# Performance work log

Measured on AMD Instinct MI355X. Metric: run time of the kernel, lower is better.

The kernel has to match this reference:

```python
import jax, jax.numpy as jnp
import numpy as np

TAU = 0.05
SIGMA = 0.05
THETA = 1.0
MAX_ITER = 30
B, N, M1, M2 = 8192, 256, 128, 64


def setup_inputs() -> dict:
    key = jax.random.key(0)
    k = jax.random.split(key, 5)
    x0 = jax.random.normal(k[0], (B, N), dtype=jnp.float32)
    y1_0 = jnp.zeros((B, M1), dtype=jnp.float32)
    y2_0 = jnp.zeros((B, M2), dtype=jnp.float32)
    z = jax.random.normal(k[1], (B, M1 + M2), dtype=jnp.float32)
    c = jax.random.normal(k[2], (N,), dtype=jnp.float32)
    # scale constraint matrices so tau*sigma*||A||^2 < 1 (PDHG stability)
    A1 = jax.random.normal(k[3], (M1, N), dtype=jnp.float32) * 0.1
    A2 = jax.random.normal(k[4], (M2, N), dtype=jnp.float32) * 0.1
    return {"x0": x0, "y1_0": y1_0, "y2_0": y2_0, "z": z, "c": c, "A1": A1, "A2": A2}


def reference(x0, y1_0, y2_0, z, c, A1, A2):
    # affine constraint maps: ineq_map(x, z) = x @ A1^T - z1 ; eq_map(x, z) = x @ A2^T - z2
    # adjoints: A1^T y1 = y1 @ A1 ; A2^T y2 = y2 @ A2
    # prox: projection onto nonnegative orthant
    z1, z2 = z[:, :M1], z[:, M1:]

    def step(carry, _):
        x, x_bar, y1, y2 = carry
        y1 = jnp.maximum(y1 + SIGMA * (x_bar @ A1.T - z1), 0.0)   # dual ineq ascent + clamp
        y2 = y2 + SIGMA * (x_bar @ A2.T - z2)                     # dual eq ascent
        grad = c + y1 @ A1 + y2 @ A2                              # [B, N] via broadcast of c
        x_next = jnp.maximum(x - TAU * grad, 0.0)                 # prox (nonneg projection)
        x_bar = x_next + THETA * (x_next - x)                     # extrapolation
        return (x_next, x_bar, y1, y2), None

    (x, _, y1, y2), _ = jax.lax.scan(step, (x0, x0, y1_0, y2_0), None, length=MAX_ITER)
    return (x, y1, y2)
```

## Files before the change

### kernel.cpp

```cpp
#include <hip/hip_runtime.h>

typedef __attribute__((ext_vector_type(8))) __bf16 bf16x8;
typedef __attribute__((ext_vector_type(4))) float f32x4;

constexpr int Bn = 8192, Nn = 256, M1n = 128, M2n = 64, Mn = 192, ITERS = 30;
constexpr float TAUc = 0.05f, SIGc = 0.05f;

__device__ __forceinline__ ushort f2bf(float f) {
  unsigned u = __builtin_bit_cast(unsigned, f);
  u = (u + 0x7FFFu + ((u >> 16) & 1u)) >> 16;
  return (ushort)u;
}

__device__ __forceinline__ unsigned cvtpk(float lo, float hi) {
  unsigned r;
  asm("v_cvt_pk_bf16_f32 %0, %1, %2" : "=v"(r) : "v"(lo), "v"(hi));
  return r;
}

__global__ void prep_kernel(const float* __restrict__ A1, const float* __restrict__ A2,
                            ushort* __restrict__ Arm, ushort* __restrict__ AT) {
  int i = blockIdx.x * 256 + threadIdx.x;
  if (i >= Mn * Nn) return;
  int m = i / Nn, n = i % Nn;
  float v = (m < M1n) ? A1[m * Nn + n] : A2[(m - M1n) * Nn + n];
  ushort b = f2bf(v);
  Arm[m * Nn + n] = b;
  AT[n * Mn + m] = b;
}

__global__ __launch_bounds__(256, 2) void pdhg_kernel(
    const float* __restrict__ x0, const float* __restrict__ y10,
    const float* __restrict__ y20, const float* __restrict__ z,
    const float* __restrict__ c, const ushort* __restrict__ Arm,
    const ushort* __restrict__ AT, float* __restrict__ out) {
  __shared__ __align__(16) ushort xb_lds[16][264];
  __shared__ __align__(16) ushort y_lds[16][200];
  __shared__ __align__(16) float z_lds[16][200];

  const int lane = threadIdx.x & 63;
  const int w = threadIdx.x >> 6;
  const int fr = lane & 15;
  const int kg = lane >> 4;
  const int row0 = blockIdx.x * 16;

  for (int idx = threadIdx.x; idx < 16 * Mn; idx += 256) {
    int r = idx / Mn, m = idx - r * Mn;
    z_lds[r][m] = SIGc * z[(row0 + r) * Mn + m];
  }

  float x[4][4], cv[4], ys[3][4];

#pragma unroll
  for (int t = 0; t < 4; ++t) {
    int n = (4 * w + t) * 16 + fr;
    cv[t] = c[n];
#pragma unroll
    for (int g = 0; g < 4; ++g) {
      float v = x0[(row0 + kg * 4 + g) * Nn + n];
      x[t][g] = v;
      xb_lds[kg * 4 + g][n] = f2bf(v);
    }
  }
#pragma unroll
  for (int i = 0; i < 3; ++i) {
    int mt = 3 * w + i;
    int m = mt * 16 + fr;
#pragma unroll
    for (int g = 0; g < 4; ++g) {
      int r = row0 + kg * 4 + g;
      ys[i][g] = (m < M1n) ? y10[r * M1n + m] : y20[r * M2n + (m - M1n)];
    }
  }

  bf16x8 armF[3][8], atF[4][6];
#pragma unroll
  for (int i = 0; i < 3; ++i) {
    int m = (3 * w + i) * 16 + fr;
#pragma unroll
    for (int kf = 0; kf < 8; ++kf)
      armF[i][kf] = *reinterpret_cast<const bf16x8*>(&Arm[m * Nn + kf * 32 + kg * 8]);
  }
#pragma unroll
  for (int t = 0; t < 4; ++t) {
    int n = (4 * w + t) * 16 + fr;
#pragma unroll
    for (int kf = 0; kf < 6; ++kf)
      atF[t][kf] = *reinterpret_cast<const bf16x8*>(&AT[n * Mn + kf * 32 + kg * 8]);
  }

  __syncthreads();

  for (int it = 0; it < ITERS; ++it) {
    f32x4 a0 = {0.f, 0.f, 0.f, 0.f}, a1 = a0, a2 = a0;
#pragma unroll
    for (int kf = 0; kf < 8; ++kf) {
      bf16x8 fx = *reinterpret_cast<const bf16x8*>(&xb_lds[fr][kf * 32 + kg * 8]);
      a0 = __builtin_amdgcn_mfma_f32_16x16x32_bf16(fx, armF[0][kf], a0, 0, 0, 0);
      a1 = __builtin_amdgcn_mfma_f32_16x16x32_bf16(fx, armF[1][kf], a1, 0, 0, 0);
      a2 = __builtin_amdgcn_mfma_f32_16x16x32_bf16(fx, armF[2][kf], a2, 0, 0, 0);
    }

#pragma unroll
    for (int i = 0; i < 3; ++i) {
      int mt = 3 * w + i;
      int m = mt * 16 + fr;
      const f32x4 ai = (i == 0) ? a0 : (i == 1) ? a1 : a2;
#pragma unroll
      for (int g = 0; g < 4; ++g) {
        float s = __builtin_fmaf(SIGc, ai[g], ys[i][g]) - z_lds[kg * 4 + g][m];
        if (mt < 8) s = fmaxf(s, 0.f);
        ys[i][g] = s;
      }
      unsigned p01 = cvtpk(ys[i][0], ys[i][1]);
      unsigned p23 = cvtpk(ys[i][2], ys[i][3]);
      y_lds[kg * 4 + 0][m] = (ushort)p01;
      y_lds[kg * 4 + 1][m] = (ushort)(p01 >> 16);
      y_lds[kg * 4 + 2][m] = (ushort)p23;
      y_lds[kg * 4 + 3][m] = (ushort)(p23 >> 16);
    }
    __syncthreads();

    f32x4 b0 = {0.f, 0.f, 0.f, 0.f}, b1 = b0, b2 = b0, b3 = b0;
#pragma unroll
    for (int kf = 0; kf < 6; ++kf) {
      bf16x8 fy = *reinterpret_cast<const bf16x8*>(&y_lds[fr][kf * 32 + kg * 8]);
      b0 = __builtin_amdgcn_mfma_f32_16x16x32_bf16(fy, atF[0][kf], b0, 0, 0, 0);
      b1 = __builtin_amdgcn_mfma_f32_16x16x32_bf16(fy, atF[1][kf], b1, 0, 0, 0);
      b2 = __builtin_amdgcn_mfma_f32_16x16x32_bf16(fy, atF[2][kf], b2, 0, 0, 0);
      b3 = __builtin_amdgcn_mfma_f32_16x16x32_bf16(fy, atF[3][kf], b3, 0, 0, 0);
    }

    const bool notlast = (it != ITERS - 1);
#pragma unroll
    for (int t = 0; t < 4; ++t) {
      int n = (4 * w + t) * 16 + fr;
      const f32x4 bt = (t == 0) ? b0 : (t == 1) ? b1 : (t == 2) ? b2 : b3;
      float xb[4];
#pragma unroll
      for (int g = 0; g < 4; ++g) {
        float grad = cv[t] + bt[g];
        float xn = fmaxf(__builtin_fmaf(-TAUc, grad, x[t][g]), 0.f);
        xb[g] = 2.f * xn - x[t][g];
        x[t][g] = xn;
      }
      if (notlast) {
        unsigned p01 = cvtpk(xb[0], xb[1]);
        unsigned p23 = cvtpk(xb[2], xb[3]);
        xb_lds[kg * 4 + 0][n] = (ushort)p01;
        xb_lds[kg * 4 + 1][n] = (ushort)(p01 >> 16);
        xb_lds[kg * 4 + 2][n] = (ushort)p23;
        xb_lds[kg * 4 + 3][n] = (ushort)(p23 >> 16);
      }
    }
    if (notlast) __syncthreads();
  }

  float* ox = out;
  float* oy1 = out + Bn * Nn;
  float* oy2 = oy1 + Bn * M1n;
#pragma unroll
  for (int t = 0; t < 4; ++t) {
    int n = (4 * w + t) * 16 + fr;
#pragma unroll
    for (int g = 0; g < 4; ++g)
      ox[(row0 + kg * 4 + g) * Nn + n] = x[t][g];
  }
#pragma unroll
  for (int i = 0; i < 3; ++i) {
    int m = (3 * w + i) * 16 + fr;
#pragma unroll
    for (int g = 0; g < 4; ++g) {
      int r = row0 + kg * 4 + g;
      if (m < M1n) oy1[r * M1n + m] = ys[i][g];
      else         oy2[r * M2n + (m - M1n)] = ys[i][g];
    }
  }
}

extern "C" void kernel_launch(void* const* d_in, const int* in_sizes, int n_in,
                              void* d_out, int out_size, void* d_ws, size_t ws_size,
                              hipStream_t stream) {
  const float* x0  = (const float*)d_in[0];
  const float* y10 = (const float*)d_in[1];
  const float* y20 = (const float*)d_in[2];
  const float* z   = (const float*)d_in[3];
  const float* c   = (const float*)d_in[4];
  const float* A1  = (const float*)d_in[5];
  const float* A2  = (const float*)d_in[6];

  ushort* Arm = (ushort*)d_ws;
  ushort* AT  = Arm + Mn * Nn;

  prep_kernel<<<(Mn * Nn + 255) / 256, 256, 0, stream>>>(A1, A2, Arm, AT);
  pdhg_kernel<<<Bn / 16, 256, 0, stream>>>(x0, y10, y20, z, c, Arm, AT, (float*)d_out);
}
```

Measured before the change: 81.81 us.

## Process two 16-row batches per block with matrix fragments pinned in AGPRs

Each block now handles 32 batch rows as two 16-row sub-tiles that share the register-resident A and A^T fragments, halving the number of blocks and the per-block fragment loads. The fragments are forced into accumulation registers through inline asm, and MFMAs take their B operand from AGPRs, freeing VGPRs for the doubled x/y state. Issuing two independent MFMA streams per barrier phase gives more instruction-level parallelism, but occupancy drops to one block per CU and only 256 blocks remain, which may underfill the GPU.

```diff
diff --git a/kernel.cpp b/kernel.cpp
--- a/kernel.cpp
+++ b/kernel.cpp
@@ -2,6 +2,7 @@
 
 typedef __attribute__((ext_vector_type(8))) __bf16 bf16x8;
 typedef __attribute__((ext_vector_type(4))) float f32x4;
+typedef __attribute__((ext_vector_type(4))) int i32x4;
 
 constexpr int Bn = 8192, Nn = 256, M1n = 128, M2n = 64, Mn = 192, ITERS = 30;
 constexpr float TAUc = 0.05f, SIGc = 0.05f;
@@ -16,6 +17,12 @@
   unsigned r;
   asm("v_cvt_pk_bf16_f32 %0, %1, %2" : "=v"(r) : "v"(lo), "v"(hi));
   return r;
+}
+
+__device__ __forceinline__ void pina(i32x4& v) { asm volatile("" : "+a"(v)); }
+
+__device__ __forceinline__ void mfma_ab(f32x4& acc, bf16x8 a, i32x4 b) {
+  asm("v_mfma_f32_16x16x32_bf16 %0, %1, %2, %0" : "+v"(acc) : "v"(a), "a"(b));
 }
 
 __global__ void prep_kernel(const float* __restrict__ A1, const float* __restrict__ A2,
@@ -29,128 +36,160 @@
   AT[n * Mn + m] = b;
 }
 
-__global__ __launch_bounds__(256, 2) void pdhg_kernel(
+__global__ __launch_bounds__(256, 1) void pdhg_kernel(
     const float* __restrict__ x0, const float* __restrict__ y10,
     const float* __restrict__ y20, const float* __restrict__ z,
     const float* __restrict__ c, const ushort* __restrict__ Arm,
     const ushort* __restrict__ AT, float* __restrict__ out) {
-  __shared__ __align__(16) ushort xb_lds[16][264];
-  __shared__ __align__(16) ushort y_lds[16][200];
-  __shared__ __align__(16) float z_lds[16][200];
+  __shared__ __align__(16) ushort xb_lds[2][16][264];
+  __shared__ __align__(16) ushort y_lds[2][16][200];
+  __shared__ float z_lds[32][201];
 
   const int lane = threadIdx.x & 63;
   const int w = threadIdx.x >> 6;
   const int fr = lane & 15;
   const int kg = lane >> 4;
-  const int row0 = blockIdx.x * 16;
-
-  for (int idx = threadIdx.x; idx < 16 * Mn; idx += 256) {
+  const int row0 = blockIdx.x * 32;
+
+  for (int idx = threadIdx.x; idx < 32 * Mn; idx += 256) {
     int r = idx / Mn, m = idx - r * Mn;
     z_lds[r][m] = SIGc * z[(row0 + r) * Mn + m];
   }
 
-  float x[4][4], cv[4], ys[3][4];
+  float x[2][4][4], cv[4], ys[2][3][4];
 
 #pragma unroll
   for (int t = 0; t < 4; ++t) {
     int n = (4 * w + t) * 16 + fr;
     cv[t] = c[n];
 #pragma unroll
-    for (int g = 0; g < 4; ++g) {
-      float v = x0[(row0 + kg * 4 + g) * Nn + n];
-      x[t][g] = v;
-      xb_lds[kg * 4 + g][n] = f2bf(v);
-    }
-  }
-#pragma unroll
-  for (int i = 0; i < 3; ++i) {
-    int mt = 3 * w + i;
-    int m = mt * 16 + fr;
-#pragma unroll
-    for (int g = 0; g < 4; ++g) {
-      int r = row0 + kg * 4 + g;
-      ys[i][g] = (m < M1n) ? y10[r * M1n + m] : y20[r * M2n + (m - M1n)];
-    }
-  }
-
-  bf16x8 armF[3][8], atF[4][6];
+    for (int b = 0; b < 2; ++b)
+#pragma unroll
+      for (int g = 0; g < 4; ++g) {
+        float v = x0[(row0 + 16 * b + kg * 4 + g) * Nn + n];
+        x[b][t][g] = v;
+        xb_lds[b][kg * 4 + g][n] = f2bf(v);
+      }
+  }
 #pragma unroll
   for (int i = 0; i < 3; ++i) {
     int m = (3 * w + i) * 16 + fr;
 #pragma unroll
-    for (int kf = 0; kf < 8; ++kf)
-      armF[i][kf] = *reinterpret_cast<const bf16x8*>(&Arm[m * Nn + kf * 32 + kg * 8]);
+    for (int b = 0; b < 2; ++b)
+#pragma unroll
+      for (int g = 0; g < 4; ++g) {
+        int r = row0 + 16 * b + kg * 4 + g;
+        ys[b][i][g] = (m < M1n) ? y10[r * M1n + m] : y20[r * M2n + (m - M1n)];
+      }
+  }
+
+  i32x4 armF[3][8], atF[4][6];
+#pragma unroll
+  for (int i = 0; i < 3; ++i) {
+    int m = (3 * w + i) * 16 + fr;
+#pragma unroll
+    for (int kf = 0; kf < 8; ++kf) {
+      armF[i][kf] = *reinterpret_cast<const i32x4*>(&Arm[m * Nn + kf * 32 + kg * 8]);
+      pina(armF[i][kf]);
+    }
   }
 #pragma unroll
   for (int t = 0; t < 4; ++t) {
     int n = (4 * w + t) * 16 + fr;
 #pragma unroll
-    for (int kf = 0; kf < 6; ++kf)
-      atF[t][kf] = *reinterpret_cast<const bf16x8*>(&AT[n * Mn + kf * 32 + kg * 8]);
+    for (int kf = 0; kf < 6; ++kf) {
+      atF[t][kf] = *reinterpret_cast<const i32x4*>(&AT[n * Mn + kf * 32 + kg * 8]);
+      pina(atF[t][kf]);
+    }
   }
 
   __syncthreads();
 
   for (int it = 0; it < ITERS; ++it) {
-    f32x4 a0 = {0.f, 0.f, 0.f, 0.f}, a1 = a0, a2 = a0;
-#pragma unroll
-    for (int kf = 0; kf < 8; ++kf) {
-      bf16x8 fx = *reinterpret_cast<const bf16x8*>(&xb_lds[fr][kf * 32 + kg * 8]);
-      a0 = __builtin_amdgcn_mfma_f32_16x16x32_bf16(fx, armF[0][kf], a0, 0, 0, 0);
-      a1 = __builtin_amdgcn_mfma_f32_16x16x32_bf16(fx, armF[1][kf], a1, 0, 0, 0);
-      a2 = __builtin_amdgcn_mfma_f32_16x16x32_bf16(fx, armF[2][kf], a2, 0, 0, 0);
-    }
+    bf16x8 fx[2][8];
+#pragma unroll
+    for (int b = 0; b < 2; ++b)
+#pragma unroll
+      for (int kf = 0; kf < 8; ++kf)
+        fx[b][kf] = *reinterpret_cast<const bf16x8*>(&xb_lds[b][fr][kf * 32 + kg * 8]);
+
+    f32x4 accA[2][3];
+#pragma unroll
+    for (int b = 0; b < 2; ++b)
+#pragma unroll
+      for (int i = 0; i < 3; ++i) accA[b][i] = f32x4{0.f, 0.f, 0.f, 0.f};
+#pragma unroll
+    for (int kf = 0; kf < 8; ++kf)
+#pragma unroll
+      for (int b = 0; b < 2; ++b)
+#pragma unroll
+        for (int i = 0; i < 3; ++i)
+          mfma_ab(accA[b][i], fx[b][kf], armF[i][kf]);
 
 #pragma unroll
     for (int i = 0; i < 3; ++i) {
       int mt = 3 * w + i;
       int m = mt * 16 + fr;
-      const f32x4 ai = (i == 0) ? a0 : (i == 1) ? a1 : a2;
-#pragma unroll
-      for (int g = 0; g < 4; ++g) {
-        float s = __builtin_fmaf(SIGc, ai[g], ys[i][g]) - z_lds[kg * 4 + g][m];
-        if (mt < 8) s = fmaxf(s, 0.f);
-        ys[i][g] = s;
-      }
-      unsigned p01 = cvtpk(ys[i][0], ys[i][1]);
-      unsigned p23 = cvtpk(ys[i][2], ys[i][3]);
-      y_lds[kg * 4 + 0][m] = (ushort)p01;
-      y_lds[kg * 4 + 1][m] = (ushort)(p01 >> 16);
-      y_lds[kg * 4 + 2][m] = (ushort)p23;
-      y_lds[kg * 4 + 3][m] = (ushort)(p23 >> 16);
+#pragma unroll
+      for (int b = 0; b < 2; ++b) {
+#pragma unroll
+        for (int g = 0; g < 4; ++g) {
+          float s = __builtin_fmaf(SIGc, accA[b][i][g], ys[b][i][g]) - z_lds[16 * b + kg * 4 + g][m];
+          if (mt < 8) s = fmaxf(s, 0.f);
+          ys[b][i][g] = s;
+        }
+        unsigned p01 = cvtpk(ys[b][i][0], ys[b][i][1]);
+        unsigned p23 = cvtpk(ys[b][i][2], ys[b][i][3]);
+        y_lds[b][kg * 4 + 0][m] = (ushort)p01;
+        y_lds[b][kg * 4 + 1][m] = (ushort)(p01 >> 16);
+        y_lds[b][kg * 4 + 2][m] = (ushort)p23;
+        y_lds[b][kg * 4 + 3][m] = (ushort)(p23 >> 16);
+      }
     }
     __syncthreads();
 
-    f32x4 b0 = {0.f, 0.f, 0.f, 0.f}, b1 = b0, b2 = b0, b3 = b0;
-#pragma unroll
-    for (int kf = 0; kf < 6; ++kf) {
-      bf16x8 fy = *reinterpret_cast<const bf16x8*>(&y_lds[fr][kf * 32 + kg * 8]);
-      b0 = __builtin_amdgcn_mfma_f32_16x16x32_bf16(fy, atF[0][kf], b0, 0, 0, 0);
-      b1 = __builtin_amdgcn_mfma_f32_16x16x32_bf16(fy, atF[1][kf], b1, 0, 0, 0);
-      b2 = __builtin_amdgcn_mfma_f32_16x16x32_bf16(fy, atF[2][kf], b2, 0, 0, 0);
-      b3 = __builtin_amdgcn_mfma_f32_16x16x32_bf16(fy, atF[3][kf], b3, 0, 0, 0);
-    }
+    bf16x8 fy[2][6];
+#pragma unroll
+    for (int b = 0; b < 2; ++b)
+#pragma unroll
+      for (int kf = 0; kf < 6; ++kf)
+        fy[b][kf] = *reinterpret_cast<const bf16x8*>(&y_lds[b][fr][kf * 32 + kg * 8]);
+
+    f32x4 accB[2][4];
+#pragma unroll
+    for (int b = 0; b < 2; ++b)
+#pragma unroll
+      for (int t = 0; t < 4; ++t) accB[b][t] = f32x4{0.f, 0.f, 0.f, 0.f};
+#pragma unroll
+    for (int kf = 0; kf < 6; ++kf)
+#pragma unroll
+      for (int b = 0; b < 2; ++b)
+#pragma unroll
+        for (int t = 0; t < 4; ++t)
+          mfma_ab(accB[b][t], fy[b][kf], atF[t][kf]);
 
     const bool notlast = (it != ITERS - 1);
 #pragma unroll
     for (int t = 0; t < 4; ++t) {
       int n = (4 * w + t) * 16 + fr;
-      const f32x4 bt = (t == 0) ? b0 : (t == 1) ? b1 : (t == 2) ? b2 : b3;
-      float xb[4];
-#pragma unroll
-      for (int g = 0; g < 4; ++g) {
-        float grad = cv[t] + bt[g];
-        float xn = fmaxf(__builtin_fmaf(-TAUc, grad, x[t][g]), 0.f);
-        xb[g] = 2.f * xn - x[t][g];
-        x[t][g] = xn;
-      }
-      if (notlast) {
-        unsigned p01 = cvtpk(xb[0], xb[1]);
-        unsigned p23 = cvtpk(xb[2], xb[3]);
-        xb_lds[kg * 4 + 0][n] = (ushort)p01;
-        xb_lds[kg * 4 + 1][n] = (ushort)(p01 >> 16);
-        xb_lds[kg * 4 + 2][n] = (ushort)p23;
-        xb_lds[kg * 4 + 3][n] = (ushort)(p23 >> 16);
+#pragma unroll
+      for (int b = 0; b < 2; ++b) {
+        float xb[4];
+#pragma unroll
+        for (int g = 0; g < 4; ++g) {
+          float grad = cv[t] + accB[b][t][g];
+          float xn = fmaxf(__builtin_fmaf(-TAUc, grad, x[b][t][g]), 0.f);
+          xb[g] = 2.f * xn - x[b][t][g];
+          x[b][t][g] = xn;
+        }
+        if (notlast) {
+          unsigned p01 = cvtpk(xb[0], xb[1]);
+          unsigned p23 = cvtpk(xb[2], xb[3]);
+          xb_lds[b][kg * 4 + 0][n] = (ushort)p01;
+          xb_lds[b][kg * 4 + 1][n] = (ushort)(p01 >> 16);
+          xb_lds[b][kg * 4 + 2][n] = (ushort)p23;
+          xb_lds[b][kg * 4 + 3][n] = (ushort)(p23 >> 16);
+        }
       }
     }
     if (notlast) __syncthreads();
@@ -163,18 +202,22 @@
   for (int t = 0; t < 4; ++t) {
     int n = (4 * w + t) * 16 + fr;
 #pragma unroll
-    for (int g = 0; g < 4; ++g)
-      ox[(row0 + kg * 4 + g) * Nn + n] = x[t][g];
+    for (int b = 0; b < 2; ++b)
+#pragma unroll
+      for (int g = 0; g < 4; ++g)
+        ox[(row0 + 16 * b + kg * 4 + g) * Nn + n] = x[b][t][g];
   }
 #pragma unroll
   for (int i = 0; i < 3; ++i) {
     int m = (3 * w + i) * 16 + fr;
 #pragma unroll
-    for (int g = 0; g < 4; ++g) {
-      int r = row0 + kg * 4 + g;
-      if (m < M1n) oy1[r * M1n + m] = ys[i][g];
-      else         oy2[r * M2n + (m - M1n)] = ys[i][g];
-    }
+    for (int b = 0; b < 2; ++b)
+#pragma unroll
+      for (int g = 0; g < 4; ++g) {
+        int r = row0 + 16 * b + kg * 4 + g;
+        if (m < M1n) oy1[r * M1n + m] = ys[b][i][g];
+        else         oy2[r * M2n + (m - M1n)] = ys[b][i][g];
+      }
   }
 }
 
@@ -193,5 +236,5 @@
   ushort* AT  = Arm + Mn * Nn;
 
   prep_kernel<<<(Mn * Nn + 255) / 256, 256, 0, stream>>>(A1, A2, Arm, AT);
-  pdhg_kernel<<<Bn / 16, 256, 0, stream>>>(x0, y10, y20, z, c, Arm, AT, (float*)d_out);
-}
+  pdhg_kernel<<<Bn / 32, 256, 0, stream>>>(x0, y10, y20, z, c, Arm, AT, (float*)d_out);
+}
```

Result: slower. 86.30 us (+5.5%).

## Process 32 rows per 512-thread block and pin A fragments in AGPRs

Applied to the files above, without the earlier changes.

Each block now handles two 16-row batch tiles with 8 waves, so each wave owns fewer output tiles and reuses its register-resident A fragments across both tiles. The scaled z values move from LDS into registers, and the A fragments are pinned to AGPRs through empty inline asm to ease VGPR pressure. The aim is more waves per CU and less per-wave register load, so MFMA work and the per-iteration barriers are better hidden. The cost is half as many blocks (256), each synchronizing 512 threads every iteration. The equality part of y is split so each wave covers one tile and one batch half.

```diff
diff --git a/kernel.cpp b/kernel.cpp
--- a/kernel.cpp
+++ b/kernel.cpp
@@ -2,6 +2,7 @@
 
 typedef __attribute__((ext_vector_type(8))) __bf16 bf16x8;
 typedef __attribute__((ext_vector_type(4))) float f32x4;
+typedef __attribute__((ext_vector_type(4))) int i32x4;
 
 constexpr int Bn = 8192, Nn = 256, M1n = 128, M2n = 64, Mn = 192, ITERS = 30;
 constexpr float TAUc = 0.05f, SIGc = 0.05f;
@@ -16,6 +17,13 @@
   unsigned r;
   asm("v_cvt_pk_bf16_f32 %0, %1, %2" : "=v"(r) : "v"(lo), "v"(hi));
   return r;
+}
+
+__device__ __forceinline__ void pina(i32x4& v) { asm volatile("" : "+a"(v)); }
+
+__device__ __forceinline__ f32x4 mfma_b(bf16x8 a, i32x4 bfrag, f32x4 acc) {
+  return __builtin_amdgcn_mfma_f32_16x16x32_bf16(
+      a, __builtin_bit_cast(bf16x8, bfrag), acc, 0, 0, 0);
 }
 
 __global__ void prep_kernel(const float* __restrict__ A1, const float* __restrict__ A2,
@@ -29,64 +37,62 @@
   AT[n * Mn + m] = b;
 }
 
-__global__ __launch_bounds__(256, 2) void pdhg_kernel(
+__global__ __launch_bounds__(512, 2) void pdhg_kernel(
     const float* __restrict__ x0, const float* __restrict__ y10,
     const float* __restrict__ y20, const float* __restrict__ z,
     const float* __restrict__ c, const ushort* __restrict__ Arm,
     const ushort* __restrict__ AT, float* __restrict__ out) {
-  __shared__ __align__(16) ushort xb_lds[16][264];
-  __shared__ __align__(16) ushort y_lds[16][200];
-  __shared__ __align__(16) float z_lds[16][200];
+  __shared__ __align__(16) ushort xb_lds[2][16][264];
+  __shared__ __align__(16) ushort y_lds[2][16][200];
 
   const int lane = threadIdx.x & 63;
   const int w = threadIdx.x >> 6;
   const int fr = lane & 15;
   const int kg = lane >> 4;
-  const int row0 = blockIdx.x * 16;
-
-  for (int idx = threadIdx.x; idx < 16 * Mn; idx += 256) {
-    int r = idx / Mn, m = idx - r * Mn;
-    z_lds[r][m] = SIGc * z[(row0 + r) * Mn + m];
-  }
-
-  float x[4][4], cv[4], ys[3][4];
-
-#pragma unroll
-  for (int t = 0; t < 4; ++t) {
-    int n = (4 * w + t) * 16 + fr;
-    cv[t] = c[n];
-#pragma unroll
-    for (int g = 0; g < 4; ++g) {
-      float v = x0[(row0 + kg * 4 + g) * Nn + n];
-      x[t][g] = v;
-      xb_lds[kg * 4 + g][n] = f2bf(v);
-    }
-  }
-#pragma unroll
-  for (int i = 0; i < 3; ++i) {
-    int mt = 3 * w + i;
-    int m = mt * 16 + fr;
-#pragma unroll
-    for (int g = 0; g < 4; ++g) {
-      int r = row0 + kg * 4 + g;
-      ys[i][g] = (m < M1n) ? y10[r * M1n + m] : y20[r * M2n + (m - M1n)];
-    }
-  }
-
-  bf16x8 armF[3][8], atF[4][6];
-#pragma unroll
-  for (int i = 0; i < 3; ++i) {
-    int m = (3 * w + i) * 16 + fr;
-#pragma unroll
-    for (int kf = 0; kf < 8; ++kf)
-      armF[i][kf] = *reinterpret_cast<const bf16x8*>(&Arm[m * Nn + kf * 32 + kg * 8]);
-  }
-#pragma unroll
-  for (int t = 0; t < 4; ++t) {
-    int n = (4 * w + t) * 16 + fr;
-#pragma unroll
-    for (int kf = 0; kf < 6; ++kf)
-      atF[t][kf] = *reinterpret_cast<const bf16x8*>(&AT[n * Mn + kf * 32 + kg * 8]);
+  const int row0 = blockIdx.x * 32;
+
+  const int m01 = w * 16 + fr;
+  const int m2 = M1n + (w & 3) * 16 + fr;
+  const int bu2 = w >> 2;
+  const int nA = (2 * w) * 16 + fr;
+  const int nB = (2 * w + 1) * 16 + fr;
+
+  float x[2][2][4];
+  float yu[3][4], zu[3][4];
+  const float cvA = c[nA], cvB = c[nB];
+
+#pragma unroll
+  for (int t = 0; t < 2; ++t) {
+    const int n = t ? nB : nA;
+#pragma unroll
+    for (int b = 0; b < 2; ++b)
+#pragma unroll
+      for (int g = 0; g < 4; ++g) {
+        float v = x0[(row0 + 16 * b + kg * 4 + g) * Nn + n];
+        x[t][b][g] = v;
+        xb_lds[b][kg * 4 + g][n] = f2bf(v);
+      }
+  }
+#pragma unroll
+  for (int g = 0; g < 4; ++g) {
+    int r0 = row0 + kg * 4 + g;
+    int r1 = r0 + 16;
+    int r2 = row0 + 16 * bu2 + kg * 4 + g;
+    zu[0][g] = SIGc * z[r0 * Mn + m01];  yu[0][g] = y10[r0 * M1n + m01];
+    zu[1][g] = SIGc * z[r1 * Mn + m01];  yu[1][g] = y10[r1 * M1n + m01];
+    zu[2][g] = SIGc * z[r2 * Mn + m2];   yu[2][g] = y20[r2 * M2n + (m2 - M1n)];
+  }
+
+  i32x4 armF01[8], armF2[8], atFA[6], atFB[6];
+#pragma unroll
+  for (int kf = 0; kf < 8; ++kf) {
+    armF01[kf] = *reinterpret_cast<const i32x4*>(&Arm[m01 * Nn + kf * 32 + kg * 8]); pina(armF01[kf]);
+    armF2[kf]  = *reinterpret_cast<const i32x4*>(&Arm[m2 * Nn + kf * 32 + kg * 8]);  pina(armF2[kf]);
+  }
+#pragma unroll
+  for (int kf = 0; kf < 6; ++kf) {
+    atFA[kf] = *reinterpret_cast<const i32x4*>(&AT[nA * Mn + kf * 32 + kg * 8]); pina(atFA[kf]);
+    atFB[kf] = *reinterpret_cast<const i32x4*>(&AT[nB * Mn + kf * 32 + kg * 8]); pina(atFB[kf]);
   }
 
   __syncthreads();
@@ -95,62 +101,77 @@
     f32x4 a0 = {0.f, 0.f, 0.f, 0.f}, a1 = a0, a2 = a0;
 #pragma unroll
     for (int kf = 0; kf < 8; ++kf) {
-      bf16x8 fx = *reinterpret_cast<const bf16x8*>(&xb_lds[fr][kf * 32 + kg * 8]);
-      a0 = __builtin_amdgcn_mfma_f32_16x16x32_bf16(fx, armF[0][kf], a0, 0, 0, 0);
-      a1 = __builtin_amdgcn_mfma_f32_16x16x32_bf16(fx, armF[1][kf], a1, 0, 0, 0);
-      a2 = __builtin_amdgcn_mfma_f32_16x16x32_bf16(fx, armF[2][kf], a2, 0, 0, 0);
-    }
-
-#pragma unroll
-    for (int i = 0; i < 3; ++i) {
-      int mt = 3 * w + i;
-      int m = mt * 16 + fr;
-      const f32x4 ai = (i == 0) ? a0 : (i == 1) ? a1 : a2;
-#pragma unroll
-      for (int g = 0; g < 4; ++g) {
-        float s = __builtin_fmaf(SIGc, ai[g], ys[i][g]) - z_lds[kg * 4 + g][m];
-        if (mt < 8) s = fmaxf(s, 0.f);
-        ys[i][g] = s;
-      }
-      unsigned p01 = cvtpk(ys[i][0], ys[i][1]);
-      unsigned p23 = cvtpk(ys[i][2], ys[i][3]);
-      y_lds[kg * 4 + 0][m] = (ushort)p01;
-      y_lds[kg * 4 + 1][m] = (ushort)(p01 >> 16);
-      y_lds[kg * 4 + 2][m] = (ushort)p23;
-      y_lds[kg * 4 + 3][m] = (ushort)(p23 >> 16);
+      bf16x8 f0 = *reinterpret_cast<const bf16x8*>(&xb_lds[0][fr][kf * 32 + kg * 8]);
+      bf16x8 f1 = *reinterpret_cast<const bf16x8*>(&xb_lds[1][fr][kf * 32 + kg * 8]);
+      bf16x8 f2 = *reinterpret_cast<const bf16x8*>(&xb_lds[bu2][fr][kf * 32 + kg * 8]);
+      a0 = mfma_b(f0, armF01[kf], a0);
+      a1 = mfma_b(f1, armF01[kf], a1);
+      a2 = mfma_b(f2, armF2[kf], a2);
+    }
+
+#pragma unroll
+    for (int g = 0; g < 4; ++g) {
+      yu[0][g] = fmaxf(__builtin_fmaf(SIGc, a0[g], yu[0][g]) - zu[0][g], 0.f);
+      yu[1][g] = fmaxf(__builtin_fmaf(SIGc, a1[g], yu[1][g]) - zu[1][g], 0.f);
+      yu[2][g] = __builtin_fmaf(SIGc, a2[g], yu[2][g]) - zu[2][g];
+    }
+    {
+      unsigned p01 = cvtpk(yu[0][0], yu[0][1]), p23 = cvtpk(yu[0][2], yu[0][3]);
+      y_lds[0][kg * 4 + 0][m01] = (ushort)p01;
+      y_lds[0][kg * 4 + 1][m01] = (ushort)(p01 >> 16);
+      y_lds[0][kg * 4 + 2][m01] = (ushort)p23;
+      y_lds[0][kg * 4 + 3][m01] = (ushort)(p23 >> 16);
+    }
+    {
+      unsigned p01 = cvtpk(yu[1][0], yu[1][1]), p23 = cvtpk(yu[1][2], yu[1][3]);
+      y_lds[1][kg * 4 + 0][m01] = (ushort)p01;
+      y_lds[1][kg * 4 + 1][m01] = (ushort)(p01 >> 16);
+      y_lds[1][kg * 4 + 2][m01] = (ushort)p23;
+      y_lds[1][kg * 4 + 3][m01] = (ushort)(p23 >> 16);
+    }
+    {
+      unsigned p01 = cvtpk(yu[2][0], yu[2][1]), p23 = cvtpk(yu[2][2], yu[2][3]);
+      y_lds[bu2][kg * 4 + 0][m2] = (ushort)p01;
+      y_lds[bu2][kg * 4 + 1][m2] = (ushort)(p01 >> 16);
+      y_lds[bu2][kg * 4 + 2][m2] = (ushort)p23;
+      y_lds[bu2][kg * 4 + 3][m2] = (ushort)(p23 >> 16);
     }
     __syncthreads();
 
-    f32x4 b0 = {0.f, 0.f, 0.f, 0.f}, b1 = b0, b2 = b0, b3 = b0;
+    f32x4 b00 = {0.f, 0.f, 0.f, 0.f}, b01 = b00, b10 = b00, b11 = b00;
 #pragma unroll
     for (int kf = 0; kf < 6; ++kf) {
-      bf16x8 fy = *reinterpret_cast<const bf16x8*>(&y_lds[fr][kf * 32 + kg * 8]);
-      b0 = __builtin_amdgcn_mfma_f32_16x16x32_bf16(fy, atF[0][kf], b0, 0, 0, 0);
-      b1 = __builtin_amdgcn_mfma_f32_16x16x32_bf16(fy, atF[1][kf], b1, 0, 0, 0);
-      b2 = __builtin_amdgcn_mfma_f32_16x16x32_bf16(fy, atF[2][kf], b2, 0, 0, 0);
-      b3 = __builtin_amdgcn_mfma_f32_16x16x32_bf16(fy, atF[3][kf], b3, 0, 0, 0);
+      bf16x8 g0 = *reinterpret_cast<const bf16x8*>(&y_lds[0][fr][kf * 32 + kg * 8]);
+      bf16x8 g1 = *reinterpret_cast<const bf16x8*>(&y_lds[1][fr][kf * 32 + kg * 8]);
+      b00 = mfma_b(g0, atFA[kf], b00);
+      b01 = mfma_b(g0, atFB[kf], b01);
+      b10 = mfma_b(g1, atFA[kf], b10);
+      b11 = mfma_b(g1, atFB[kf], b11);
     }
 
     const bool notlast = (it != ITERS - 1);
 #pragma unroll
-    for (int t = 0; t < 4; ++t) {
-      int n = (4 * w + t) * 16 + fr;
-      const f32x4 bt = (t == 0) ? b0 : (t == 1) ? b1 : (t == 2) ? b2 : b3;
-      float xb[4];
-#pragma unroll
-      for (int g = 0; g < 4; ++g) {
-        float grad = cv[t] + bt[g];
-        float xn = fmaxf(__builtin_fmaf(-TAUc, grad, x[t][g]), 0.f);
-        xb[g] = 2.f * xn - x[t][g];
-        x[t][g] = xn;
-      }
-      if (notlast) {
-        unsigned p01 = cvtpk(xb[0], xb[1]);
-        unsigned p23 = cvtpk(xb[2], xb[3]);
-        xb_lds[kg * 4 + 0][n] = (ushort)p01;
-        xb_lds[kg * 4 + 1][n] = (ushort)(p01 >> 16);
-        xb_lds[kg * 4 + 2][n] = (ushort)p23;
-        xb_lds[kg * 4 + 3][n] = (ushort)(p23 >> 16);
+    for (int t = 0; t < 2; ++t) {
+      const int n = t ? nB : nA;
+      const float cv = t ? cvB : cvA;
+#pragma unroll
+      for (int b = 0; b < 2; ++b) {
+        const f32x4 bt = (t == 0) ? (b == 0 ? b00 : b10) : (b == 0 ? b01 : b11);
+        float xb[4];
+#pragma unroll
+        for (int g = 0; g < 4; ++g) {
+          float grad = cv + bt[g];
+          float xn = fmaxf(__builtin_fmaf(-TAUc, grad, x[t][b][g]), 0.f);
+          xb[g] = 2.f * xn - x[t][b][g];
+          x[t][b][g] = xn;
+        }
+        if (notlast) {
+          unsigned p01 = cvtpk(xb[0], xb[1]), p23 = cvtpk(xb[2], xb[3]);
+          xb_lds[b][kg * 4 + 0][n] = (ushort)p01;
+          xb_lds[b][kg * 4 + 1][n] = (ushort)(p01 >> 16);
+          xb_lds[b][kg * 4 + 2][n] = (ushort)p23;
+          xb_lds[b][kg * 4 + 3][n] = (ushort)(p23 >> 16);
+        }
       }
     }
     if (notlast) __syncthreads();
@@ -160,21 +181,20 @@
   float* oy1 = out + Bn * Nn;
   float* oy2 = oy1 + Bn * M1n;
 #pragma unroll
-  for (int t = 0; t < 4; ++t) {
-    int n = (4 * w + t) * 16 + fr;
-#pragma unroll
-    for (int g = 0; g < 4; ++g)
-      ox[(row0 + kg * 4 + g) * Nn + n] = x[t][g];
-  }
-#pragma unroll
-  for (int i = 0; i < 3; ++i) {
-    int m = (3 * w + i) * 16 + fr;
-#pragma unroll
-    for (int g = 0; g < 4; ++g) {
-      int r = row0 + kg * 4 + g;
-      if (m < M1n) oy1[r * M1n + m] = ys[i][g];
-      else         oy2[r * M2n + (m - M1n)] = ys[i][g];
-    }
+  for (int t = 0; t < 2; ++t) {
+    const int n = t ? nB : nA;
+#pragma unroll
+    for (int b = 0; b < 2; ++b)
+#pragma unroll
+      for (int g = 0; g < 4; ++g)
+        ox[(row0 + 16 * b + kg * 4 + g) * Nn + n] = x[t][b][g];
+  }
+#pragma unroll
+  for (int g = 0; g < 4; ++g) {
+    int r0 = row0 + kg * 4 + g;
+    oy1[r0 * M1n + m01] = yu[0][g];
+    oy1[(r0 + 16) * M1n + m01] = yu[1][g];
+    oy2[(row0 + 16 * bu2 + kg * 4 + g) * M2n + (m2 - M1n)] = yu[2][g];
   }
 }
 
@@ -193,5 +213,5 @@
   ushort* AT  = Arm + Mn * Nn;
 
   prep_kernel<<<(Mn * Nn + 255) / 256, 256, 0, stream>>>(A1, A2, Arm, AT);
-  pdhg_kernel<<<Bn / 16, 256, 0, stream>>>(x0, y10, y20, z, c, Arm, AT, (float*)d_out);
-}
+  pdhg_kernel<<<Bn / 32, 512, 0, stream>>>(x0, y10, y20, z, c, Arm, AT, (float*)d_out);
+}
```

Result: faster. 74.13 us (-9.4%).
